# Performance work log

Measured on AMD Instinct MI355X. Metric: run time of the kernel, lower is better.

The kernel has to match this reference:

```python
import jax, jax.numpy as jnp
import numpy as np

HID = 16
EMB = 32


def _cell_step(W_f, b_f, W_i, b_i, W_C, b_C, W_o, b_o):
    def step(carry, w):
        h, C = carry  # [B,H] each
        comb = jnp.concatenate([w, h], axis=1)  # [B, EMB+HID]
        f = jax.nn.sigmoid(comb @ W_f.T + b_f)
        i = jax.nn.sigmoid(comb @ W_i.T + b_i)
        C_t = jnp.tanh(comb @ W_C.T + b_C)
        C_new = f * C + i * C_t
        o = jax.nn.sigmoid(comb @ W_o.T + b_o)
        h_new = o * jnp.tanh(C_new)
        return (h_new, C_new), h_new
    return step


def setup_inputs() -> dict:
    key = jax.random.key(0)
    ks = jax.random.split(key, 16)
    V, S, B = 50257, 64, 32
    stdv = 1.0 / np.sqrt(HID)
    u = lambda k, shape: jax.random.uniform(k, shape, jnp.float32, -stdv, stdv)
    return {
        "input_batch": jax.random.randint(ks[0], (S, B), 0, V),
        "embedding": jax.random.normal(ks[1], (V, EMB), jnp.float32),
        "W_f": u(ks[2], (HID, EMB + HID)), "b_f": u(ks[3], (HID,)),
        "W_i": u(ks[4], (HID, EMB + HID)), "b_i": u(ks[5], (HID,)),
        "W_C": u(ks[6], (HID, EMB + HID)), "b_C": u(ks[7], (HID,)),
        "W_o": u(ks[8], (HID, EMB + HID)), "b_o": u(ks[9], (HID,)),
        "W_ho": u(ks[10], (V, 2 * HID)), "b_ho": u(ks[11], (V,)),
        "initial_hidden": u(ks[12], (1, HID)),
        "initial_C": u(ks[13], (1, HID)),
    }


def reference(input_batch, embedding, W_f, b_f, W_i, b_i, W_C, b_C, W_o, b_o,
              W_ho, b_ho, initial_hidden, initial_C):
    S, B = input_batch.shape
    emb = embedding[input_batch]  # [S,B,EMB]
    h0 = jnp.broadcast_to(initial_hidden, (B, HID))
    C0 = jnp.broadcast_to(initial_C, (B, HID))
    step = _cell_step(W_f, b_f, W_i, b_i, W_C, b_C, W_o, b_o)

    # Left-to-right: hLR[t] = hidden after consuming inputs[0..t-1]; hLR[0]=h0
    _, hL_out = jax.lax.scan(step, (h0, C0), emb)
    lefts = jnp.concatenate([h0[None], hL_out[:-1]], axis=0)  # hLR[i], i=0..S-1

    # Right-to-left over reversed sequence (shared cell weights, same init)
    _, r_out = jax.lax.scan(step, (h0, C0), emb[::-1])
    flipped = r_out[::-1]  # flipped[m] = hidden after consuming input[m]
    # prediction i uses hRL[i+2]: output after consuming input[i+1] (init for i=S-1)
    rights = jnp.concatenate([flipped[1:], h0[None]], axis=0)

    concat_h = jnp.concatenate([lefts, rights], axis=-1)  # [S,B,2H]
    logits = jnp.einsum('sbh,vh->sbv', concat_h, W_ho) + b_ho
    return jax.nn.log_softmax(logits, axis=-1)
```

## Files before the change

### kernel.cpp

```cpp
#include <hip/hip_runtime.h>
#include <hip/hip_bf16.h>
#include <math.h>

constexpr int S   = 64;
constexpr int B   = 32;
constexpr int HID = 16;
constexpr int EMB = 32;
constexpr int V   = 50257;
constexpr int CH  = 2*HID;
constexpr int IN  = EMB + HID;
constexpr int VPAD = 50272;
constexpr int NT32 = VPAD/32;
constexpr int MT32 = (S*B)/32;
constexpr int NSTRIP = 32;
constexpr int NT_PER = (NT32 + NSTRIP - 1)/NSTRIP;
constexpr int NB_CONV = (VPAD*CH)/256;
constexpr int NB_XW   = (S*B)/4;

typedef __attribute__((ext_vector_type(8)))  short bf16x8;
typedef __attribute__((ext_vector_type(16))) float f32x16;

__device__ inline float sigm(float x)      { return 1.f/(1.f + __expf(-x)); }
__device__ inline float tanh_fast(float x) { return 1.f - 2.f/(1.f + __expf(2.f*x)); }

__global__ __launch_bounds__(256) void kprep(
    const int* __restrict__ tok, const float* __restrict__ emb,
    const float* __restrict__ Wf, const float* __restrict__ bf,
    const float* __restrict__ Wi, const float* __restrict__ bi,
    const float* __restrict__ Wc, const float* __restrict__ bc,
    const float* __restrict__ Wo, const float* __restrict__ bo,
    const float* __restrict__ Who, const float* __restrict__ bho,
    __hip_bfloat16* __restrict__ WhoB, float* __restrict__ bhoP,
    float* __restrict__ xw, float* __restrict__ row_sums)
{
    int bid = blockIdx.x, t = threadIdx.x;
    if (bid < NB_CONV) {
        int i = bid*256 + t;
        int r = i >> 5;
        WhoB[i] = __float2bfloat16((r < V) ? Who[i] : 0.f);
        if (i < VPAD) bhoP[i] = (i < V) ? bho[i] : -30.f;
        if (i < S*B)  row_sums[i] = 0.f;
    } else {
        int grp = t >> 6, lane = t & 63;
        int sb  = (bid - NB_CONV)*4 + grp;
        __shared__ float e[4][EMB];
        if (lane < EMB) e[grp][lane] = emb[(long)tok[sb]*EMB + lane];
        __syncthreads();
        int g = lane >> 4, h = lane & 15;
        const float* W  = (g==0) ? Wf : (g==1) ? Wi : (g==2) ? Wc : Wo;
        const float* bv = (g==0) ? bf : (g==1) ? bi : (g==2) ? bc : bo;
        const float* wr = W + h*IN;
        float acc = bv[h];
        #pragma unroll
        for (int k = 0; k < EMB; ++k) acc += e[grp][k]*wr[k];
        xw[sb*64 + lane] = acc;
    }
}

__global__ __launch_bounds__(64) void k2_scan(
    const float* __restrict__ xw,
    const float* __restrict__ Wf, const float* __restrict__ Wi,
    const float* __restrict__ Wc, const float* __restrict__ Wo,
    const float* __restrict__ h0, const float* __restrict__ C0,
    __hip_bfloat16* __restrict__ hcatB)
{
    int id  = blockIdx.x;
    int dir = id >> 5, b = id & 31;
    int lane = threadIdx.x;
    int g = lane >> 4, hh = lane & 15;
    const float* W = (g==0) ? Wf : (g==1) ? Wi : (g==2) ? Wc : Wo;
    float U[HID];
    #pragma unroll
    for (int k = 0; k < HID; ++k) U[k] = W[hh*IN + EMB + k];
    float h = h0[hh], C = C0[hh];
    int sb     = dir ? (S-1)*B + b : b;
    int stride = dir ? -B : B;
    float xn = xw[sb*64 + lane];
    for (int step = 0; step < S; ++step) {
        float p = xn;
        if (step + 1 < S) xn = xw[(sb + stride)*64 + lane];
        if (g == 0) hcatB[sb*CH + dir*HID + hh] = __float2bfloat16(h);
        float q0 = 0.f, q1 = 0.f, q2 = 0.f, q3 = 0.f;
        #pragma unroll
        for (int k = 0; k < HID; k += 4) {
            q0 += U[k  ]*__shfl(h, k,   64);
            q1 += U[k+1]*__shfl(h, k+1, 64);
            q2 += U[k+2]*__shfl(h, k+2, 64);
            q3 += U[k+3]*__shfl(h, k+3, 64);
        }
        p += (q0+q1) + (q2+q3);
        float a = (g==2) ? tanh_fast(p) : sigm(p);
        float fg = __shfl(a,      hh, 64);
        float ig = __shfl(a, 16 + hh, 64);
        float cg = __shfl(a, 32 + hh, 64);
        float og = __shfl(a, 48 + hh, 64);
        C = fg*C + ig*cg;
        h = og*tanh_fast(C);
        sb += stride;
    }
}

__global__ __launch_bounds__(256) void kA(
    const __hip_bfloat16* __restrict__ hcatB, const __hip_bfloat16* __restrict__ WhoB,
    const float* __restrict__ bhoP, float* __restrict__ row_sums)
{
    int t = threadIdx.x, w = t >> 6, lane = t & 63;
    int l31 = lane & 31, half = lane >> 5;
    int r0 = (blockIdx.y*4 + w)*32;
    int n0 = blockIdx.x*NT_PER;
    int n1 = (n0 + NT_PER < NT32) ? n0 + NT_PER : NT32;
    const short* hp = (const short*)hcatB + (r0 + l31)*CH + half*8;
    bf16x8 a0 = *(const bf16x8*)hp;
    bf16x8 a1 = *(const bf16x8*)(hp + 16);
    float acc[16];
    #pragma unroll
    for (int r = 0; r < 16; ++r) acc[r] = 0.f;
    for (int nt = n0; nt < n1; ++nt) {
        int v0 = nt*32;
        const short* bp = (const short*)WhoB + (long)(v0 + l31)*CH + half*8;
        bf16x8 b0 = *(const bf16x8*)bp;
        bf16x8 b1 = *(const bf16x8*)(bp + 16);
        float bv = bhoP[v0 + l31];
        f32x16 d;
        #pragma unroll
        for (int r = 0; r < 16; ++r) d[r] = bv;
        d = __builtin_amdgcn_mfma_f32_32x32x16_bf16(a0, b0, d, 0, 0, 0);
        d = __builtin_amdgcn_mfma_f32_32x32x16_bf16(a1, b1, d, 0, 0, 0);
        #pragma unroll
        for (int r = 0; r < 16; ++r) acc[r] += __expf(d[r]);
    }
    #pragma unroll
    for (int off = 1; off < 32; off <<= 1) {
        #pragma unroll
        for (int r = 0; r < 16; ++r) acc[r] += __shfl_xor(acc[r], off);
    }
    if (l31 == 0) {
        #pragma unroll
        for (int r = 0; r < 16; ++r)
            atomicAdd(&row_sums[r0 + (r&3) + 8*(r>>2) + 4*half], acc[r]);
    }
}

__global__ __launch_bounds__(256) void kB(
    const __hip_bfloat16* __restrict__ hcatB, const __hip_bfloat16* __restrict__ WhoB,
    const float* __restrict__ bhoP, const float* __restrict__ row_sums,
    float* __restrict__ out)
{
    int t = threadIdx.x, w = t >> 6, lane = t & 63;
    int l31 = lane & 31, half = lane >> 5;
    int r0 = (blockIdx.y*4 + w)*32;
    int n0 = blockIdx.x*NT_PER;
    int n1 = (n0 + NT_PER < NT32) ? n0 + NT_PER : NT32;
    const short* hp = (const short*)hcatB + (r0 + l31)*CH + half*8;
    bf16x8 a0 = *(const bf16x8*)hp;
    bf16x8 a1 = *(const bf16x8*)(hp + 16);
    float    lzr[16];
    unsigned obase[16];
    #pragma unroll
    for (int r = 0; r < 16; ++r) {
        int row = r0 + (r&3) + 8*(r>>2) + 4*half;
        lzr[r]   = logf(row_sums[row]);
        obase[r] = (unsigned)row*V + l31;
    }
    for (int nt = n0; nt < n1; ++nt) {
        int v0 = nt*32;
        const short* bp = (const short*)WhoB + (long)(v0 + l31)*CH + half*8;
        bf16x8 b0 = *(const bf16x8*)bp;
        bf16x8 b1 = *(const bf16x8*)(bp + 16);
        float bv = bhoP[v0 + l31];
        f32x16 d;
        #pragma unroll
        for (int r = 0; r < 16; ++r) d[r] = bv - lzr[r];
        d = __builtin_amdgcn_mfma_f32_32x32x16_bf16(a0, b0, d, 0, 0, 0);
        d = __builtin_amdgcn_mfma_f32_32x32x16_bf16(a1, b1, d, 0, 0, 0);
        if (v0 + l31 < V) {
            #pragma unroll
            for (int r = 0; r < 16; ++r) out[obase[r] + v0] = d[r];
        }
    }
}

extern "C" void kernel_launch(void* const* d_in, const int* in_sizes, int n_in,
                              void* d_out, int out_size, void* d_ws, size_t ws_size,
                              hipStream_t stream)
{
    const int*   tok = (const int*)d_in[0];
    const float* emb = (const float*)d_in[1];
    const float* Wf  = (const float*)d_in[2];
    const float* bf  = (const float*)d_in[3];
    const float* Wi  = (const float*)d_in[4];
    const float* bi  = (const float*)d_in[5];
    const float* Wc  = (const float*)d_in[6];
    const float* bc  = (const float*)d_in[7];
    const float* Wo  = (const float*)d_in[8];
    const float* bo  = (const float*)d_in[9];
    const float* Who = (const float*)d_in[10];
    const float* bho = (const float*)d_in[11];
    const float* h0  = (const float*)d_in[12];
    const float* C0  = (const float*)d_in[13];
    float* out = (float*)d_out;

    char* p = (char*)d_ws;
    __hip_bfloat16* WhoB  = (__hip_bfloat16*)p; p += (size_t)VPAD*CH*2;
    __hip_bfloat16* hcatB = (__hip_bfloat16*)p; p += (size_t)S*B*CH*2;
    float* bhoP     = (float*)p; p += (size_t)VPAD*4;
    float* xw       = (float*)p; p += (size_t)S*B*64*4;
    float* row_sums = (float*)p;

    kprep<<<dim3(NB_CONV + NB_XW), dim3(256), 0, stream>>>(
        tok, emb, Wf, bf, Wi, bi, Wc, bc, Wo, bo, Who, bho,
        WhoB, bhoP, xw, row_sums);
    k2_scan<<<dim3(64), dim3(64), 0, stream>>>(xw, Wf, Wi, Wc, Wo, h0, C0, hcatB);
    dim3 g(NSTRIP, MT32/4);
    kA<<<g, dim3(256), 0, stream>>>(hcatB, WhoB, bhoP, row_sums);
    kB<<<g, dim3(256), 0, stream>>>(hcatB, WhoB, bhoP, row_sums, out);
}
```

Before: 622.9 us.

## Interleave both scan directions per block, prefetch weights, widen vocab split, nontemporal stores

The recurrent scan now runs both directions in one wavefront per batch element, using readlane broadcasts and rcp-based sigmoid/tanh to shorten the serial dependency chain. The logits kernels software-prefetch the next W_ho tile and bias, double the vocabulary strip count for more blocks, and set occupancy hints. The output kernel writes logits with nontemporal stores to avoid polluting cache. These aim to hide load latency and raise parallelism, at the cost of more registers and half as many scan blocks.

```diff
diff --git a/kernel.cpp b/kernel.cpp
--- a/kernel.cpp
+++ b/kernel.cpp
@@ -12,7 +12,7 @@
 constexpr int VPAD = 50272;
 constexpr int NT32 = VPAD/32;
 constexpr int MT32 = (S*B)/32;
-constexpr int NSTRIP = 32;
+constexpr int NSTRIP = 64;
 constexpr int NT_PER = (NT32 + NSTRIP - 1)/NSTRIP;
 constexpr int NB_CONV = (VPAD*CH)/256;
 constexpr int NB_XW   = (S*B)/4;
@@ -20,8 +20,10 @@
 typedef __attribute__((ext_vector_type(8)))  short bf16x8;
 typedef __attribute__((ext_vector_type(16))) float f32x16;
 
-__device__ inline float sigm(float x)      { return 1.f/(1.f + __expf(-x)); }
-__device__ inline float tanh_fast(float x) { return 1.f - 2.f/(1.f + __expf(2.f*x)); }
+__device__ inline float bcast(float v, int l) {
+    return __uint_as_float(__builtin_amdgcn_readlane(__float_as_uint(v), l));
+}
+__device__ inline float rcp_fast(float x) { return __builtin_amdgcn_rcpf(x); }
 
 __global__ __launch_bounds__(256) void kprep(
     const int* __restrict__ tok, const float* __restrict__ emb,
@@ -64,43 +66,60 @@
     const float* __restrict__ h0, const float* __restrict__ C0,
     __hip_bfloat16* __restrict__ hcatB)
 {
-    int id  = blockIdx.x;
-    int dir = id >> 5, b = id & 31;
+    int b    = blockIdx.x;
     int lane = threadIdx.x;
     int g = lane >> 4, hh = lane & 15;
     const float* W = (g==0) ? Wf : (g==1) ? Wi : (g==2) ? Wc : Wo;
     float U[HID];
     #pragma unroll
     for (int k = 0; k < HID; ++k) U[k] = W[hh*IN + EMB + k];
-    float h = h0[hh], C = C0[hh];
-    int sb     = dir ? (S-1)*B + b : b;
-    int stride = dir ? -B : B;
-    float xn = xw[sb*64 + lane];
+    float hA = h0[hh], CA = C0[hh];
+    float hB = h0[hh], CB = C0[hh];
+    int sbA = b, sbB = (S-1)*B + b;
+    float xnA = xw[sbA*64 + lane];
+    float xnB = xw[sbB*64 + lane];
     for (int step = 0; step < S; ++step) {
-        float p = xn;
-        if (step + 1 < S) xn = xw[(sb + stride)*64 + lane];
-        if (g == 0) hcatB[sb*CH + dir*HID + hh] = __float2bfloat16(h);
-        float q0 = 0.f, q1 = 0.f, q2 = 0.f, q3 = 0.f;
+        float pA = xnA, pB = xnB;
+        if (step + 1 < S) {
+            xnA = xw[(sbA + B)*64 + lane];
+            xnB = xw[(sbB - B)*64 + lane];
+        }
+        if (g == 0) {
+            hcatB[sbA*CH + hh]       = __float2bfloat16(hA);
+            hcatB[sbB*CH + HID + hh] = __float2bfloat16(hB);
+        }
+        float qA0=0.f,qA1=0.f,qA2=0.f,qA3=0.f;
+        float qB0=0.f,qB1=0.f,qB2=0.f,qB3=0.f;
         #pragma unroll
         for (int k = 0; k < HID; k += 4) {
-            q0 += U[k  ]*__shfl(h, k,   64);
-            q1 += U[k+1]*__shfl(h, k+1, 64);
-            q2 += U[k+2]*__shfl(h, k+2, 64);
-            q3 += U[k+3]*__shfl(h, k+3, 64);
-        }
-        p += (q0+q1) + (q2+q3);
-        float a = (g==2) ? tanh_fast(p) : sigm(p);
-        float fg = __shfl(a,      hh, 64);
-        float ig = __shfl(a, 16 + hh, 64);
-        float cg = __shfl(a, 32 + hh, 64);
-        float og = __shfl(a, 48 + hh, 64);
-        C = fg*C + ig*cg;
-        h = og*tanh_fast(C);
-        sb += stride;
-    }
-}
-
-__global__ __launch_bounds__(256) void kA(
+            qA0 += U[k  ]*bcast(hA, k  );  qB0 += U[k  ]*bcast(hB, k  );
+            qA1 += U[k+1]*bcast(hA, k+1);  qB1 += U[k+1]*bcast(hB, k+1);
+            qA2 += U[k+2]*bcast(hA, k+2);  qB2 += U[k+2]*bcast(hB, k+2);
+            qA3 += U[k+3]*bcast(hA, k+3);  qB3 += U[k+3]*bcast(hB, k+3);
+        }
+        pA += (qA0+qA1) + (qA2+qA3);
+        pB += (qB0+qB1) + (qB2+qB3);
+        float tA = (g==2) ? pA+pA : pA;
+        float tB = (g==2) ? pB+pB : pB;
+        float eA = __expf(-tA), eB = __expf(-tB);
+        float sA = rcp_fast(1.f + eA), sB = rcp_fast(1.f + eB);
+        float aA = (g==2) ? sA+sA-1.f : sA;
+        float aB = (g==2) ? sB+sB-1.f : sB;
+        float fgA = __shfl(aA,      hh, 64), fgB = __shfl(aB,      hh, 64);
+        float igA = __shfl(aA, 16 + hh, 64), igB = __shfl(aB, 16 + hh, 64);
+        float cgA = __shfl(aA, 32 + hh, 64), cgB = __shfl(aB, 32 + hh, 64);
+        float ogA = __shfl(aA, 48 + hh, 64), ogB = __shfl(aB, 48 + hh, 64);
+        CA = fgA*CA + igA*cgA;
+        CB = fgB*CB + igB*cgB;
+        float e2A = __expf(-(CA+CA));
+        float e2B = __expf(-(CB+CB));
+        hA = ogA*(2.f*rcp_fast(1.f + e2A) - 1.f);
+        hB = ogB*(2.f*rcp_fast(1.f + e2B) - 1.f);
+        sbA += B; sbB -= B;
+    }
+}
+
+__global__ __launch_bounds__(256, 4) void kA(
     const __hip_bfloat16* __restrict__ hcatB, const __hip_bfloat16* __restrict__ WhoB,
     const float* __restrict__ bhoP, float* __restrict__ row_sums)
 {
@@ -108,6 +127,7 @@
     int l31 = lane & 31, half = lane >> 5;
     int r0 = (blockIdx.y*4 + w)*32;
     int n0 = blockIdx.x*NT_PER;
+    if (n0 >= NT32) return;
     int n1 = (n0 + NT_PER < NT32) ? n0 + NT_PER : NT32;
     const short* hp = (const short*)hcatB + (r0 + l31)*CH + half*8;
     bf16x8 a0 = *(const bf16x8*)hp;
@@ -115,12 +135,16 @@
     float acc[16];
     #pragma unroll
     for (int r = 0; r < 16; ++r) acc[r] = 0.f;
+    const short* bp = (const short*)WhoB + (long)(n0*32 + l31)*CH + half*8;
+    bf16x8 b0 = *(const bf16x8*)bp;
+    bf16x8 b1 = *(const bf16x8*)(bp + 16);
+    float  bv = bhoP[n0*32 + l31];
     for (int nt = n0; nt < n1; ++nt) {
-        int v0 = nt*32;
-        const short* bp = (const short*)WhoB + (long)(v0 + l31)*CH + half*8;
-        bf16x8 b0 = *(const bf16x8*)bp;
-        bf16x8 b1 = *(const bf16x8*)(bp + 16);
-        float bv = bhoP[v0 + l31];
+        int ntn = (nt + 1 < n1) ? nt + 1 : nt;
+        const short* bpn = (const short*)WhoB + (long)(ntn*32 + l31)*CH + half*8;
+        bf16x8 nb0 = *(const bf16x8*)bpn;
+        bf16x8 nb1 = *(const bf16x8*)(bpn + 16);
+        float  nbv = bhoP[ntn*32 + l31];
         f32x16 d;
         #pragma unroll
         for (int r = 0; r < 16; ++r) d[r] = bv;
@@ -128,6 +152,7 @@
         d = __builtin_amdgcn_mfma_f32_32x32x16_bf16(a1, b1, d, 0, 0, 0);
         #pragma unroll
         for (int r = 0; r < 16; ++r) acc[r] += __expf(d[r]);
+        b0 = nb0; b1 = nb1; bv = nbv;
     }
     #pragma unroll
     for (int off = 1; off < 32; off <<= 1) {
@@ -141,7 +166,7 @@
     }
 }
 
-__global__ __launch_bounds__(256) void kB(
+__global__ __launch_bounds__(256, 4) void kB(
     const __hip_bfloat16* __restrict__ hcatB, const __hip_bfloat16* __restrict__ WhoB,
     const float* __restrict__ bhoP, const float* __restrict__ row_sums,
     float* __restrict__ out)
@@ -150,6 +175,7 @@
     int l31 = lane & 31, half = lane >> 5;
     int r0 = (blockIdx.y*4 + w)*32;
     int n0 = blockIdx.x*NT_PER;
+    if (n0 >= NT32) return;
     int n1 = (n0 + NT_PER < NT32) ? n0 + NT_PER : NT32;
     const short* hp = (const short*)hcatB + (r0 + l31)*CH + half*8;
     bf16x8 a0 = *(const bf16x8*)hp;
@@ -162,21 +188,30 @@
         lzr[r]   = logf(row_sums[row]);
         obase[r] = (unsigned)row*V + l31;
     }
+    const short* bp = (const short*)WhoB + (long)(n0*32 + l31)*CH + half*8;
+    bf16x8 b0 = *(const bf16x8*)bp;
+    bf16x8 b1 = *(const bf16x8*)(bp + 16);
+    float  bv = bhoP[n0*32 + l31];
+    bool inV = true;
     for (int nt = n0; nt < n1; ++nt) {
         int v0 = nt*32;
-        const short* bp = (const short*)WhoB + (long)(v0 + l31)*CH + half*8;
-        bf16x8 b0 = *(const bf16x8*)bp;
-        bf16x8 b1 = *(const bf16x8*)(bp + 16);
-        float bv = bhoP[v0 + l31];
+        int ntn = (nt + 1 < n1) ? nt + 1 : nt;
+        const short* bpn = (const short*)WhoB + (long)(ntn*32 + l31)*CH + half*8;
+        bf16x8 nb0 = *(const bf16x8*)bpn;
+        bf16x8 nb1 = *(const bf16x8*)(bpn + 16);
+        float  nbv = bhoP[ntn*32 + l31];
         f32x16 d;
         #pragma unroll
         for (int r = 0; r < 16; ++r) d[r] = bv - lzr[r];
         d = __builtin_amdgcn_mfma_f32_32x32x16_bf16(a0, b0, d, 0, 0, 0);
         d = __builtin_amdgcn_mfma_f32_32x32x16_bf16(a1, b1, d, 0, 0, 0);
-        if (v0 + l31 < V) {
+        inV = (v0 + l31 < V);
+        if (inV) {
             #pragma unroll
-            for (int r = 0; r < 16; ++r) out[obase[r] + v0] = d[r];
-        }
+            for (int r = 0; r < 16; ++r)
+                __builtin_nontemporal_store(d[r], &out[obase[r] + v0]);
+        }
+        b0 = nb0; b1 = nb1; bv = nbv;
     }
 }
 
@@ -210,7 +245,7 @@
     kprep<<<dim3(NB_CONV + NB_XW), dim3(256), 0, stream>>>(
         tok, emb, Wf, bf, Wi, bi, Wc, bc, Wo, bo, Who, bho,
         WhoB, bhoP, xw, row_sums);
-    k2_scan<<<dim3(64), dim3(64), 0, stream>>>(xw, Wf, Wi, Wc, Wo, h0, C0, hcatB);
+    k2_scan<<<dim3(32), dim3(64), 0, stream>>>(xw, Wf, Wi, Wc, Wo, h0, C0, hcatB);
     dim3 g(NSTRIP, MT32/4);
     kA<<<g, dim3(256), 0, stream>>>(hcatB, WhoB, bhoP, row_sums);
     kB<<<g, dim3(256), 0, stream>>>(hcatB, WhoB, bhoP, row_sums, out);
```

Result: slower. 809.0 us (+29.9%).
